# Kernel optimization log

Measured on AMD Instinct MI355X. Metric: run time of the kernel, lower is better.

The kernel has to match this reference:

```python
import jax, jax.numpy as jnp
import numpy as np
from math import sqrt

N_HEADS = 4
IN_FEATURES = 64
KQ = 64
HEAD_V = IN_FEATURES // N_HEADS  # 16


def setup_inputs() -> dict:
    key = jax.random.key(0)
    ks = jax.random.split(key, 7)
    s = 0.05
    x = jax.random.normal(ks[0], (8192, IN_FEATURES), dtype=jnp.float32)
    # Per-head Linear weights stacked on a leading head axis.
    # torch Linear: y = x @ W.T + b; we store W already transposed: [H, F, E]
    Wq = jax.random.normal(ks[1], (N_HEADS, IN_FEATURES, KQ), dtype=jnp.float32) * s
    bq = jax.random.normal(ks[2], (N_HEADS, KQ), dtype=jnp.float32) * s
    Wk = jax.random.normal(ks[3], (N_HEADS, IN_FEATURES, KQ), dtype=jnp.float32) * s
    bk = jax.random.normal(ks[4], (N_HEADS, KQ), dtype=jnp.float32) * s
    Wv = jax.random.normal(ks[5], (N_HEADS, IN_FEATURES, HEAD_V), dtype=jnp.float32) * s
    bv = jax.random.normal(ks[6], (N_HEADS, HEAD_V), dtype=jnp.float32) * s
    return {"x": x, "Wq": Wq, "bq": bq, "Wk": Wk, "bk": bk, "Wv": Wv, "bv": bv}


def reference(x, Wq, bq, Wk, bk, Wv, bv):
    N, F = x.shape
    scale = 1.0 / sqrt(F)  # original divides by sqrt(in_features), NOT sqrt(kq)
    # Batched-head projections: [H, N, E]
    Q = jnp.einsum('nf,hfe->hne', x, Wq) + bq[:, None, :]
    K = jnp.einsum('nf,hfe->hne', x, Wk) + bk[:, None, :]
    V = jnp.einsum('nf,hfd->hnd', x, Wv) + bv[:, None, :]
    logits = jnp.einsum('hne,hme->hnm', Q, K) * scale  # [H, N, N]
    attn = jax.nn.softmax(logits, axis=-1)
    out_heads = jnp.einsum('hnm,hmd->hnd', attn, V)    # [H, N, HEAD_V]
    # Head i writes columns [i*HEAD_V:(i+1)*HEAD_V] of the output.
    out = jnp.transpose(out_heads, (1, 0, 2)).reshape(N, F)
    return out
```

## Files before the change

kernel.cpp:

```cpp
#include <hip/hip_runtime.h>

typedef __attribute__((ext_vector_type(4))) float f32x4;
typedef __attribute__((ext_vector_type(8))) short bf16x8;
typedef __attribute__((ext_vector_type(4))) short bf16x4;
typedef long fp8x8;

#define NH 4

static __device__ __forceinline__ unsigned short f2bf(float f){
  unsigned u = __float_as_uint(f);
  u += 0x7FFFu + ((u >> 16) & 1u);
  return (unsigned short)(u >> 16);
}

static __device__ __forceinline__ unsigned pack2bf(float a, float b){
  return __builtin_amdgcn_perm(__float_as_uint(b) + 0x8000u,
                               __float_as_uint(a) + 0x8000u, 0x07060302u);
}

static __device__ __forceinline__ unsigned pack2bf_t(float a, float b){
  return __builtin_amdgcn_perm(__float_as_uint(b), __float_as_uint(a), 0x07060302u);
}

static __device__ __forceinline__ int pack_fp8x4(float a, float b, float c, float d){
  int w = __builtin_amdgcn_cvt_pk_fp8_f32(a, b, 0, false);
  w     = __builtin_amdgcn_cvt_pk_fp8_f32(c, d, w, true);
  return w;
}

__global__ __launch_bounds__(256) void wprep_kernel(
    const float* __restrict__ Wq, const float* __restrict__ bq,
    const float* __restrict__ Wk, const float* __restrict__ bk,
    const float* __restrict__ Wv,
    unsigned short* __restrict__ WF, float* __restrict__ bias_s, int n)
{
  __shared__ unsigned short wqT[64*72];
  __shared__ unsigned short wkT[64*72];
  __shared__ unsigned short wvT[16*72];

  const int t = threadIdx.x;
  const int h = blockIdx.x;
  const float S1 = 0.4246609001f;
  const int f = t >> 2, eg = t & 3;

  {
    const float4* g = (const float4*)(Wq + h*4096 + f*64 + eg*16);
    #pragma unroll
    for (int p = 0; p < 4; ++p){
      float4 d = g[p];
      int e0 = eg*16 + p*4;
      wqT[(e0+0)*72 + f] = f2bf(d.x * S1);
      wqT[(e0+1)*72 + f] = f2bf(d.y * S1);
      wqT[(e0+2)*72 + f] = f2bf(d.z * S1);
      wqT[(e0+3)*72 + f] = f2bf(d.w * S1);
    }
  }
  {
    const float4* g = (const float4*)(Wk + h*4096 + f*64 + eg*16);
    #pragma unroll
    for (int p = 0; p < 4; ++p){
      float4 d = g[p];
      int e0 = eg*16 + p*4;
      wkT[(e0+0)*72 + f] = f2bf(d.x * S1);
      wkT[(e0+1)*72 + f] = f2bf(d.y * S1);
      wkT[(e0+2)*72 + f] = f2bf(d.z * S1);
      wkT[(e0+3)*72 + f] = f2bf(d.w * S1);
    }
  }
  {
    float4 d = *(const float4*)(Wv + h*1024 + f*16 + eg*4);
    int d0 = eg*4;
    wvT[(d0+0)*72 + f] = f2bf(d.x);
    wvT[(d0+1)*72 + f] = f2bf(d.y);
    wvT[(d0+2)*72 + f] = f2bf(d.z);
    wvT[(d0+3)*72 + f] = f2bf(d.w);
  }
  if (t < 64)       bias_s[h*128 + t] = bq[h*64 + t] * S1;
  else if (t < 128) bias_s[h*128 + t] = bk[h*64 + (t-64)] * S1;
  __syncthreads();

  const int lane = t & 63, w = t >> 6;
  const int quad = lane >> 4, l16 = lane & 15;
  for (int s = w; s < 18; s += 4){
    const unsigned short* src;
    if (s < 8){      int et = s>>1,     ks = s&1;     src = wqT + (et*16+l16)*72 + ks*32 + quad*8; }
    else if (s < 16){int ft = (s-8)>>1, ks = (s-8)&1; src = wkT + (ft*16+l16)*72 + ks*32 + quad*8; }
    else {           int ks = s-16;                   src = wvT + l16*72 + ks*32 + quad*8; }
    uint4 v = *(const uint4*)src;
    *(uint4*)(WF + ((size_t)(h*18 + s)*64 + lane)*8) = v;
  }
}

__global__ __launch_bounds__(256) void proj_kernel(
    const float* __restrict__ x, const float* __restrict__ bv,
    const unsigned short* __restrict__ WF, const float* __restrict__ bias_s,
    unsigned char* __restrict__ Qfr, unsigned char* __restrict__ Kt,
    unsigned short* __restrict__ Vt, int n)
{
  __shared__ unsigned short xf[8*64*8];
  __shared__ float bql[64], bkl[64], bvl[16];

  const int t  = threadIdx.x;
  const int h  = blockIdx.y;
  const int r0 = blockIdx.x * 64;

  {
    const int r = t >> 2, cg4 = t & 3;
    const float4* g = (const float4*)(x + (size_t)(r0 + r)*64 + cg4*16);
    float4 a = g[0], b = g[1], c = g[2], d = g[3];
    unsigned u0 = pack2bf(a.x,a.y), u1 = pack2bf(a.z,a.w);
    unsigned u2 = pack2bf(b.x,b.y), u3 = pack2bf(b.z,b.w);
    unsigned u4 = pack2bf(c.x,c.y), u5 = pack2bf(c.z,c.w);
    unsigned u6 = pack2bf(d.x,d.y), u7 = pack2bf(d.z,d.w);
    const int it = r >> 4, l16r = r & 15, ks = cg4 >> 1, q0 = (cg4 & 1)*2;
    uint4* dst0 = (uint4*)(xf + ((it*2+ks)*64 + q0*16     + l16r)*8);
    uint4* dst1 = (uint4*)(xf + ((it*2+ks)*64 + (q0+1)*16 + l16r)*8);
    *dst0 = make_uint4(u0,u1,u2,u3);
    *dst1 = make_uint4(u4,u5,u6,u7);
  }
  if (t < 64)        bql[t]     = bias_s[h*128 + t];
  else if (t < 128)  bkl[t-64]  = bias_s[h*128 + t];
  else if (t < 144)  bvl[t-128] = bv[h*16 + (t-128)];
  __syncthreads();

  const int lane = t & 63, w = t >> 6;
  const int quad = lane >> 4, l16 = lane & 15;

  bf16x8 xa[8];
  #pragma unroll
  for (int i = 0; i < 8; ++i)
    xa[i] = *(const bf16x8*)(xf + (i*64 + lane)*8);

  const unsigned short* WFh = WF + (size_t)h*18*64*8;
  bf16x8 wq0 = *(const bf16x8*)(WFh + ((size_t)(     w*2 + 0)*64 + lane)*8);
  bf16x8 wq1 = *(const bf16x8*)(WFh + ((size_t)(     w*2 + 1)*64 + lane)*8);
  bf16x8 wk0 = *(const bf16x8*)(WFh + ((size_t)(8  + w*2 + 0)*64 + lane)*8);
  bf16x8 wk1 = *(const bf16x8*)(WFh + ((size_t)(8  + w*2 + 1)*64 + lane)*8);
  bf16x8 wv0 = *(const bf16x8*)(WFh + ((size_t)16*64 + lane)*8);
  bf16x8 wv1 = *(const bf16x8*)(WFh + ((size_t)17*64 + lane)*8);

  const f32x4 z = {0.f,0.f,0.f,0.f};
  f32x4 accQ[4] = {z,z,z,z};
  f32x4 accK[4] = {z,z,z,z};
  f32x4 accV = z;

  #pragma unroll
  for (int it = 0; it < 4; ++it){
    accQ[it] = __builtin_amdgcn_mfma_f32_16x16x32_bf16(wq0, xa[it*2+0], accQ[it], 0,0,0);
    accQ[it] = __builtin_amdgcn_mfma_f32_16x16x32_bf16(wq1, xa[it*2+1], accQ[it], 0,0,0);
  }
  #pragma unroll
  for (int tt = 0; tt < 4; ++tt){
    accK[tt] = __builtin_amdgcn_mfma_f32_16x16x32_bf16(wk0, xa[tt*2+0], accK[tt], 0,0,0);
    accK[tt] = __builtin_amdgcn_mfma_f32_16x16x32_bf16(wk1, xa[tt*2+1], accK[tt], 0,0,0);
  }
  accV = __builtin_amdgcn_mfma_f32_16x16x32_bf16(xa[w*2+0], wv0, accV, 0,0,0);
  accV = __builtin_amdgcn_mfma_f32_16x16x32_bf16(xa[w*2+1], wv1, accV, 0,0,0);

  {
    const int e0 = w*16 + quad*4;
    const float b0 = bql[e0], b1 = bql[e0+1], b2 = bql[e0+2], b3 = bql[e0+3];
    const int qk = (e0 & 31) >> 3, hf = e0 >> 5, boff = (quad & 1) * 4;
    #pragma unroll
    for (int it = 0; it < 4; ++it){
      unsigned o = pack_fp8x4(accQ[it][0]+b0, accQ[it][1]+b1,
                              accQ[it][2]+b2, accQ[it][3]+b3);
      const int T = (r0 >> 4) + it;
      *(unsigned*)(Qfr + (size_t)h*((size_t)n<<6) + (size_t)T*1024
                       + (qk*16 + l16)*16 + hf*8 + boff) = o;
    }
  }
  {
    const int f0 = w*16 + quad*4;
    const float bk0 = bkl[f0], bk1 = bkl[f0+1], bk2 = bkl[f0+2], bk3 = bkl[f0+3];
    const int qk = (f0 & 31) >> 3, hf = f0 >> 5, boff = (quad & 1) * 4;
    #pragma unroll
    for (int tt = 0; tt < 4; ++tt){
      unsigned o = pack_fp8x4(accK[tt][0]+bk0, accK[tt][1]+bk1,
                              accK[tt][2]+bk2, accK[tt][3]+bk3);
      const int T = (r0 >> 4) + tt;
      *(unsigned*)(Kt + (size_t)h*((size_t)n<<6) + (size_t)T*1024
                      + (qk*16 + l16)*16 + hf*8 + boff) = o;
    }
  }
  {
    float bvv = bvl[l16];
    unsigned v01 = pack2bf(accV[0]+bvv, accV[1]+bvv);
    unsigned v23 = pack2bf(accV[2]+bvv, accV[3]+bvv);
    const int T = (r0 >> 4) + w;
    *(uint2*)(Vt + (size_t)h*((size_t)n<<4) + ((size_t)T*64 + lane)*4) = make_uint2(v01, v23);
  }
}

__global__ __launch_bounds__(512, 8) void attn_kernel(
    const unsigned char* __restrict__ Qfr, const unsigned char* __restrict__ Kt,
    const unsigned short* __restrict__ Vt, float* __restrict__ out, int n)
{
  __shared__ float part[7][64][17];

  const int tid  = threadIdx.x;
  const int lane = tid & 63;
  const int jq   = tid >> 6;
  const int bid  = blockIdx.x;
  const int h    = bid & 3;
  const int iblk = bid >> 2;
  const int l16  = lane & 15, quad = lane >> 4;
  const int i0   = iblk*32;
  const int ntq  = (n >> 3) >> 4;
  const int tile0 = jq * ntq;

  const unsigned char* qfh = Qfr + (size_t)h*((size_t)n<<6);
  longlong2 q0 = *(const longlong2*)(qfh + (size_t)((i0>>4)    )*1024 + lane*16);
  longlong2 q1 = *(const longlong2*)(qfh + (size_t)((i0>>4) + 1)*1024 + lane*16);
  const fp8x8 qf00 = (fp8x8)q0.x;
  const fp8x8 qf01 = (fp8x8)q0.y;
  const fp8x8 qf10 = (fp8x8)q1.x;
  const fp8x8 qf11 = (fp8x8)q1.y;

  const longlong2* ktl = (const longlong2*)(Kt + (size_t)h*((size_t)n<<6)) + (size_t)tile0*64 + lane;
  const uint2*     vtu = (const uint2*)(Vt + (size_t)h*((size_t)n<<4)) + (size_t)tile0*64 + lane;

  f32x4 o0  = {0.f,0.f,0.f,0.f};
  f32x4 o1  = {0.f,0.f,0.f,0.f};
  f32x4 la0 = {0.f,0.f,0.f,0.f};
  f32x4 la1 = {0.f,0.f,0.f,0.f};
  const f32x4 z = {0.f,0.f,0.f,0.f};
  const bf16x4 vones = {(short)0x3F80, (short)0x3F80, (short)0x3F80, (short)0x3F80};

  longlong2 ka = ktl[0];
  uint2     va = vtu[0];
  longlong2 kb = ktl[64];
  uint2     vb = vtu[64];

#define ATTN_TILE(KK, VV)                                                     \
  {                                                                           \
    fp8x8 k0 = (fp8x8)KK.x;                                                   \
    fp8x8 k1 = (fp8x8)KK.y;                                                   \
    bf16x4 vf; { union { uint2 u; bf16x4 v; } c; c.u = VV; vf = c.v; }        \
    f32x4 s0 = __builtin_amdgcn_mfma_f32_16x16x32_fp8_fp8(k0, qf00, z, 0,0,0);\
    s0 = __builtin_amdgcn_mfma_f32_16x16x32_fp8_fp8(k1, qf01, s0, 0,0,0);     \
    f32x4 s1 = __builtin_amdgcn_mfma_f32_16x16x32_fp8_fp8(k0, qf10, z, 0,0,0);\
    s1 = __builtin_amdgcn_mfma_f32_16x16x32_fp8_fp8(k1, qf11, s1, 0,0,0);     \
    float p00 = __builtin_amdgcn_exp2f(s0[0]);                                \
    float p01 = __builtin_amdgcn_exp2f(s0[1]);                                \
    float p02 = __builtin_amdgcn_exp2f(s0[2]);                                \
    float p03 = __builtin_amdgcn_exp2f(s0[3]);                                \
    float p10 = __builtin_amdgcn_exp2f(s1[0]);                                \
    float p11 = __builtin_amdgcn_exp2f(s1[1]);                                \
    float p12 = __builtin_amdgcn_exp2f(s1[2]);                                \
    float p13 = __builtin_amdgcn_exp2f(s1[3]);                                \
    union { uint2 u; bf16x4 v; } pc0, pc1;                                    \
    pc0.u = make_uint2(pack2bf_t(p00,p01), pack2bf_t(p02,p03));               \
    pc1.u = make_uint2(pack2bf_t(p10,p11), pack2bf_t(p12,p13));               \
    o0  = __builtin_amdgcn_mfma_f32_16x16x16bf16_1k(pc0.v, vf,    o0,  0,0,0);\
    o1  = __builtin_amdgcn_mfma_f32_16x16x16bf16_1k(pc1.v, vf,    o1,  0,0,0);\
    la0 = __builtin_amdgcn_mfma_f32_16x16x16bf16_1k(pc0.v, vones, la0, 0,0,0);\
    la1 = __builtin_amdgcn_mfma_f32_16x16x16bf16_1k(pc1.v, vones, la1, 0,0,0);\
  }

  for (int tt = 0; tt < ntq - 2; tt += 2){
    longlong2 kc = ktl[128];
    uint2     vc = vtu[128];
    longlong2 kd = ktl[192];
    uint2     vd = vtu[192];
    ATTN_TILE(ka, va)
    ATTN_TILE(kb, vb)
    ka = kc; va = vc;
    kb = kd; vb = vd;
    ktl += 128; vtu += 128;
  }
  ATTN_TILE(ka, va)
  ATTN_TILE(kb, vb)
#undef ATTN_TILE

  if (jq > 0){
    float* p = &part[jq-1][lane][0];
    p[ 0]=o0[0];  p[ 1]=o0[1];  p[ 2]=o0[2];  p[ 3]=o0[3];
    p[ 4]=o1[0];  p[ 5]=o1[1];  p[ 6]=o1[2];  p[ 7]=o1[3];
    p[ 8]=la0[0]; p[ 9]=la0[1]; p[10]=la0[2]; p[11]=la0[3];
    p[12]=la1[0]; p[13]=la1[1]; p[14]=la1[2]; p[15]=la1[3];
  }
  __syncthreads();

  if (jq == 0){
    #pragma unroll
    for (int q = 0; q < 7; ++q){
      const float* r = &part[q][lane][0];
      o0[0] +=r[0];  o0[1] +=r[1];  o0[2] +=r[2];  o0[3] +=r[3];
      o1[0] +=r[4];  o1[1] +=r[5];  o1[2] +=r[6];  o1[3] +=r[7];
      la0[0]+=r[8];  la0[1]+=r[9];  la0[2]+=r[10]; la0[3]+=r[11];
      la1[0]+=r[12]; la1[1]+=r[13]; la1[2]+=r[14]; la1[3]+=r[15];
    }
    #pragma unroll
    for (int reg = 0; reg < 4; ++reg){
      int i = quad*4 + reg;
      out[(size_t)(i0 + i)*64      + h*16 + l16] = o0[reg] / la0[reg];
      out[(size_t)(i0 + 16 + i)*64 + h*16 + l16] = o1[reg] / la1[reg];
    }
  }
}

extern "C" void kernel_launch(void* const* d_in, const int* in_sizes, int n_in,
                              void* d_out, int out_size, void* d_ws, size_t ws_size,
                              hipStream_t stream) {
  const float* x  = (const float*)d_in[0];
  const float* Wq = (const float*)d_in[1];
  const float* bq = (const float*)d_in[2];
  const float* Wk = (const float*)d_in[3];
  const float* bk = (const float*)d_in[4];
  const float* Wv = (const float*)d_in[5];
  const float* bv = (const float*)d_in[6];
  float* out = (float*)d_out;

  const int n = in_sizes[0] / 64;

  unsigned char* Qfr  = (unsigned char*)d_ws;
  unsigned char* Kt   = Qfr + (size_t)NH*n*64;
  unsigned short* Vt  = (unsigned short*)(Kt + (size_t)NH*n*64);
  unsigned short* WF  = Vt + (size_t)NH*n*16;
  float* bias_s       = (float*)(WF + (size_t)NH*18*64*8);

  wprep_kernel<<<NH, 256, 0, stream>>>(Wq, bq, Wk, bk, Wv, WF, bias_s, n);
  proj_kernel<<<dim3(n/64, NH), 256, 0, stream>>>(x, bv, WF, bias_s, Qfr, Kt, Vt, n);
  attn_kernel<<<dim3((n/32)*NH), 512, 0, stream>>>(Qfr, Kt, Vt, out, n);
}
```

Measured before the change: 122.4 us.

## Use 16x16x32 bf16 MFMA for PV by pairing key tiles with interleaved V layout

Stores V so that two consecutive 16-key tiles sit interleaved in one 16-byte per-lane chunk. The attention loop now handles two key tiles per step and issues the PV and row-sum products with the K=32 bf16 MFMA instead of two K=16 MFMAs. This halves the PV/rowsum MFMA instruction count and widens the V loads. It also relaxes launch bounds from 8 to 4 waves-per-EU minimum, which allows more registers per thread but may reduce occupancy. Prefetch depth in the loop changes to match the chunked schedule.

```diff
diff --git a/kernel.cpp b/kernel.cpp
--- a/kernel.cpp
+++ b/kernel.cpp
@@ -188,11 +188,12 @@
     unsigned v01 = pack2bf(accV[0]+bvv, accV[1]+bvv);
     unsigned v23 = pack2bf(accV[2]+bvv, accV[3]+bvv);
     const int T = (r0 >> 4) + w;
-    *(uint2*)(Vt + (size_t)h*((size_t)n<<4) + ((size_t)T*64 + lane)*4) = make_uint2(v01, v23);
-  }
-}
-
-__global__ __launch_bounds__(512, 8) void attn_kernel(
+    *(uint2*)(Vt + (size_t)h*((size_t)n<<4)
+                 + ((size_t)(T>>1)*64 + lane)*8 + (T&1)*4) = make_uint2(v01, v23);
+  }
+}
+
+__global__ __launch_bounds__(512, 4) void attn_kernel(
     const unsigned char* __restrict__ Qfr, const unsigned char* __restrict__ Kt,
     const unsigned short* __restrict__ Vt, float* __restrict__ out, int n)
 {
@@ -207,6 +208,7 @@
   const int l16  = lane & 15, quad = lane >> 4;
   const int i0   = iblk*32;
   const int ntq  = (n >> 3) >> 4;
+  const int nch  = ntq >> 1;
   const int tile0 = jq * ntq;
 
   const unsigned char* qfh = Qfr + (size_t)h*((size_t)n<<6);
@@ -218,60 +220,74 @@
   const fp8x8 qf11 = (fp8x8)q1.y;
 
   const longlong2* ktl = (const longlong2*)(Kt + (size_t)h*((size_t)n<<6)) + (size_t)tile0*64 + lane;
-  const uint2*     vtu = (const uint2*)(Vt + (size_t)h*((size_t)n<<4)) + (size_t)tile0*64 + lane;
+  const uint4*     vtu = (const uint4*)(Vt + (size_t)h*((size_t)n<<4)) + (size_t)(tile0>>1)*64 + lane;
 
   f32x4 o0  = {0.f,0.f,0.f,0.f};
   f32x4 o1  = {0.f,0.f,0.f,0.f};
   f32x4 la0 = {0.f,0.f,0.f,0.f};
   f32x4 la1 = {0.f,0.f,0.f,0.f};
   const f32x4 z = {0.f,0.f,0.f,0.f};
-  const bf16x4 vones = {(short)0x3F80, (short)0x3F80, (short)0x3F80, (short)0x3F80};
-
-  longlong2 ka = ktl[0];
-  uint2     va = vtu[0];
-  longlong2 kb = ktl[64];
-  uint2     vb = vtu[64];
-
-#define ATTN_TILE(KK, VV)                                                     \
+  const bf16x8 vones = {(short)0x3F80, (short)0x3F80, (short)0x3F80, (short)0x3F80,
+                        (short)0x3F80, (short)0x3F80, (short)0x3F80, (short)0x3F80};
+
+  longlong2 ka0 = ktl[0],   ka1 = ktl[64];
+  uint4     va  = vtu[0];
+  longlong2 kb0 = ktl[128], kb1 = ktl[192];
+  uint4     vb  = vtu[64];
+
+#define ATTN_CHUNK(KA, KB, VV)                                                \
   {                                                                           \
-    fp8x8 k0 = (fp8x8)KK.x;                                                   \
-    fp8x8 k1 = (fp8x8)KK.y;                                                   \
-    bf16x4 vf; { union { uint2 u; bf16x4 v; } c; c.u = VV; vf = c.v; }        \
-    f32x4 s0 = __builtin_amdgcn_mfma_f32_16x16x32_fp8_fp8(k0, qf00, z, 0,0,0);\
-    s0 = __builtin_amdgcn_mfma_f32_16x16x32_fp8_fp8(k1, qf01, s0, 0,0,0);     \
-    f32x4 s1 = __builtin_amdgcn_mfma_f32_16x16x32_fp8_fp8(k0, qf10, z, 0,0,0);\
-    s1 = __builtin_amdgcn_mfma_f32_16x16x32_fp8_fp8(k1, qf11, s1, 0,0,0);     \
-    float p00 = __builtin_amdgcn_exp2f(s0[0]);                                \
-    float p01 = __builtin_amdgcn_exp2f(s0[1]);                                \
-    float p02 = __builtin_amdgcn_exp2f(s0[2]);                                \
-    float p03 = __builtin_amdgcn_exp2f(s0[3]);                                \
-    float p10 = __builtin_amdgcn_exp2f(s1[0]);                                \
-    float p11 = __builtin_amdgcn_exp2f(s1[1]);                                \
-    float p12 = __builtin_amdgcn_exp2f(s1[2]);                                \
-    float p13 = __builtin_amdgcn_exp2f(s1[3]);                                \
-    union { uint2 u; bf16x4 v; } pc0, pc1;                                    \
-    pc0.u = make_uint2(pack2bf_t(p00,p01), pack2bf_t(p02,p03));               \
-    pc1.u = make_uint2(pack2bf_t(p10,p11), pack2bf_t(p12,p13));               \
-    o0  = __builtin_amdgcn_mfma_f32_16x16x16bf16_1k(pc0.v, vf,    o0,  0,0,0);\
-    o1  = __builtin_amdgcn_mfma_f32_16x16x16bf16_1k(pc1.v, vf,    o1,  0,0,0);\
-    la0 = __builtin_amdgcn_mfma_f32_16x16x16bf16_1k(pc0.v, vones, la0, 0,0,0);\
-    la1 = __builtin_amdgcn_mfma_f32_16x16x16bf16_1k(pc1.v, vones, la1, 0,0,0);\
-  }
-
-  for (int tt = 0; tt < ntq - 2; tt += 2){
-    longlong2 kc = ktl[128];
-    uint2     vc = vtu[128];
-    longlong2 kd = ktl[192];
-    uint2     vd = vtu[192];
-    ATTN_TILE(ka, va)
-    ATTN_TILE(kb, vb)
-    ka = kc; va = vc;
-    kb = kd; vb = vd;
-    ktl += 128; vtu += 128;
-  }
-  ATTN_TILE(ka, va)
-  ATTN_TILE(kb, vb)
-#undef ATTN_TILE
+    fp8x8 a0 = (fp8x8)KA.x;                                                   \
+    fp8x8 a1 = (fp8x8)KA.y;                                                   \
+    fp8x8 b0 = (fp8x8)KB.x;                                                   \
+    fp8x8 b1 = (fp8x8)KB.y;                                                   \
+    f32x4 s0 = __builtin_amdgcn_mfma_f32_16x16x32_fp8_fp8(a0, qf00, z, 0,0,0);\
+    s0 = __builtin_amdgcn_mfma_f32_16x16x32_fp8_fp8(a1, qf01, s0, 0,0,0);     \
+    f32x4 s1 = __builtin_amdgcn_mfma_f32_16x16x32_fp8_fp8(a0, qf10, z, 0,0,0);\
+    s1 = __builtin_amdgcn_mfma_f32_16x16x32_fp8_fp8(a1, qf11, s1, 0,0,0);     \
+    f32x4 t0 = __builtin_amdgcn_mfma_f32_16x16x32_fp8_fp8(b0, qf00, z, 0,0,0);\
+    t0 = __builtin_amdgcn_mfma_f32_16x16x32_fp8_fp8(b1, qf01, t0, 0,0,0);     \
+    f32x4 t1 = __builtin_amdgcn_mfma_f32_16x16x32_fp8_fp8(b0, qf10, z, 0,0,0);\
+    t1 = __builtin_amdgcn_mfma_f32_16x16x32_fp8_fp8(b1, qf11, t1, 0,0,0);     \
+    float pa00 = __builtin_amdgcn_exp2f(s0[0]);                               \
+    float pa01 = __builtin_amdgcn_exp2f(s0[1]);                               \
+    float pa02 = __builtin_amdgcn_exp2f(s0[2]);                               \
+    float pa03 = __builtin_amdgcn_exp2f(s0[3]);                               \
+    float pa10 = __builtin_amdgcn_exp2f(s1[0]);                               \
+    float pa11 = __builtin_amdgcn_exp2f(s1[1]);                               \
+    float pa12 = __builtin_amdgcn_exp2f(s1[2]);                               \
+    float pa13 = __builtin_amdgcn_exp2f(s1[3]);                               \
+    float pb00 = __builtin_amdgcn_exp2f(t0[0]);                               \
+    float pb01 = __builtin_amdgcn_exp2f(t0[1]);                               \
+    float pb02 = __builtin_amdgcn_exp2f(t0[2]);                               \
+    float pb03 = __builtin_amdgcn_exp2f(t0[3]);                               \
+    float pb10 = __builtin_amdgcn_exp2f(t1[0]);                               \
+    float pb11 = __builtin_amdgcn_exp2f(t1[1]);                               \
+    float pb12 = __builtin_amdgcn_exp2f(t1[2]);                               \
+    float pb13 = __builtin_amdgcn_exp2f(t1[3]);                               \
+    union { uint4 u; bf16x8 v; } pq0, pq1, vfu;                               \
+    pq0.u = make_uint4(pack2bf_t(pa00,pa01), pack2bf_t(pa02,pa03),            \
+                       pack2bf_t(pb00,pb01), pack2bf_t(pb02,pb03));           \
+    pq1.u = make_uint4(pack2bf_t(pa10,pa11), pack2bf_t(pa12,pa13),            \
+                       pack2bf_t(pb10,pb11), pack2bf_t(pb12,pb13));           \
+    vfu.u = VV;                                                               \
+    o0  = __builtin_amdgcn_mfma_f32_16x16x32_bf16(pq0.v, vfu.v, o0,  0,0,0);  \
+    o1  = __builtin_amdgcn_mfma_f32_16x16x32_bf16(pq1.v, vfu.v, o1,  0,0,0);  \
+    la0 = __builtin_amdgcn_mfma_f32_16x16x32_bf16(pq0.v, vones, la0, 0,0,0);  \
+    la1 = __builtin_amdgcn_mfma_f32_16x16x32_bf16(pq1.v, vones, la1, 0,0,0);  \
+  }
+
+  for (int c = 0; c < nch - 2; ++c){
+    longlong2 kc0 = ktl[256], kc1 = ktl[320];
+    uint4     vc  = vtu[128];
+    ATTN_CHUNK(ka0, ka1, va)
+    ka0 = kb0; ka1 = kb1; va = vb;
+    kb0 = kc0; kb1 = kc1; vb = vc;
+    ktl += 128; vtu += 64;
+  }
+  ATTN_CHUNK(ka0, ka1, va)
+  ATTN_CHUNK(kb0, kb1, vb)
+#undef ATTN_CHUNK
 
   if (jq > 0){
     float* p = &part[jq-1][lane][0];
```

New measurement: 120.8 us. No clear change (-1.3%).

## Split attention into MFMA and exp2 warp roles with LDS ping-pong pipeline

Applied to the files above, without the earlier changes.

Attention is restructured into warp specialization. Four waves run the QK fp8 MFMAs and the PV bf16 MFMAs, and four other waves run exp2 and bf16 packing. Scores and probabilities pass between them through double-buffered, swizzled LDS with a block barrier each chunk. V is stored interleaved so PV can use the 16x16x32 bf16 MFMA. Occupancy hint drops from 8 to 4 and the cross-wave reduction shrinks to 2 partials. The goal is to overlap transcendental work with matrix work, at the cost of per-chunk __syncthreads and LDS traffic.

```diff
diff --git a/kernel.cpp b/kernel.cpp
--- a/kernel.cpp
+++ b/kernel.cpp
@@ -2,7 +2,6 @@
 
 typedef __attribute__((ext_vector_type(4))) float f32x4;
 typedef __attribute__((ext_vector_type(8))) short bf16x8;
-typedef __attribute__((ext_vector_type(4))) short bf16x4;
 typedef long fp8x8;
 
 #define NH 4
@@ -188,114 +187,139 @@
     unsigned v01 = pack2bf(accV[0]+bvv, accV[1]+bvv);
     unsigned v23 = pack2bf(accV[2]+bvv, accV[3]+bvv);
     const int T = (r0 >> 4) + w;
-    *(uint2*)(Vt + (size_t)h*((size_t)n<<4) + ((size_t)T*64 + lane)*4) = make_uint2(v01, v23);
-  }
-}
-
-__global__ __launch_bounds__(512, 8) void attn_kernel(
+    *(uint2*)(Vt + (size_t)h*((size_t)n<<4)
+                 + ((size_t)(T>>1)*64 + lane)*8 + (T&1)*4) = make_uint2(v01, v23);
+  }
+}
+
+__global__ __launch_bounds__(512, 4) void attn_kernel(
     const unsigned char* __restrict__ Qfr, const unsigned char* __restrict__ Kt,
     const unsigned short* __restrict__ Vt, float* __restrict__ out, int n)
 {
-  __shared__ float part[7][64][17];
+  __shared__ char xbuf[16384 + 8192];
+  __shared__ float part[2][64][9];
+
+  char* sbv = xbuf;
+  char* pbv = xbuf + 16384;
 
   const int tid  = threadIdx.x;
   const int lane = tid & 63;
-  const int jq   = tid >> 6;
+  const int w    = tid >> 6;
+  const bool mw  = (w < 4);
+  const int p    = w & 3;
+  const int rh   = p & 1;
+  const int kh   = p >> 1;
+
   const int bid  = blockIdx.x;
   const int h    = bid & 3;
   const int iblk = bid >> 2;
   const int l16  = lane & 15, quad = lane >> 4;
   const int i0   = iblk*32;
-  const int ntq  = (n >> 3) >> 4;
-  const int tile0 = jq * ntq;
-
-  const unsigned char* qfh = Qfr + (size_t)h*((size_t)n<<6);
-  longlong2 q0 = *(const longlong2*)(qfh + (size_t)((i0>>4)    )*1024 + lane*16);
-  longlong2 q1 = *(const longlong2*)(qfh + (size_t)((i0>>4) + 1)*1024 + lane*16);
-  const fp8x8 qf00 = (fp8x8)q0.x;
-  const fp8x8 qf01 = (fp8x8)q0.y;
-  const fp8x8 qf10 = (fp8x8)q1.x;
-  const fp8x8 qf11 = (fp8x8)q1.y;
-
-  const longlong2* ktl = (const longlong2*)(Kt + (size_t)h*((size_t)n<<6)) + (size_t)tile0*64 + lane;
-  const uint2*     vtu = (const uint2*)(Vt + (size_t)h*((size_t)n<<4)) + (size_t)tile0*64 + lane;
-
-  f32x4 o0  = {0.f,0.f,0.f,0.f};
-  f32x4 o1  = {0.f,0.f,0.f,0.f};
-  f32x4 la0 = {0.f,0.f,0.f,0.f};
-  f32x4 la1 = {0.f,0.f,0.f,0.f};
+  const int nch  = n >> 6;
+  const int tile0 = kh * (n >> 5);
+
+  const int swz = (lane*16) ^ (((lane>>3)&3) << 4);
+  char* sbp = sbv + p*2048 + swz;
+  char* pbp = pbv + p*1024 + swz;
+
   const f32x4 z = {0.f,0.f,0.f,0.f};
-  const bf16x4 vones = {(short)0x3F80, (short)0x3F80, (short)0x3F80, (short)0x3F80};
-
-  longlong2 ka = ktl[0];
-  uint2     va = vtu[0];
-  longlong2 kb = ktl[64];
-  uint2     vb = vtu[64];
-
-#define ATTN_TILE(KK, VV)                                                     \
-  {                                                                           \
-    fp8x8 k0 = (fp8x8)KK.x;                                                   \
-    fp8x8 k1 = (fp8x8)KK.y;                                                   \
-    bf16x4 vf; { union { uint2 u; bf16x4 v; } c; c.u = VV; vf = c.v; }        \
-    f32x4 s0 = __builtin_amdgcn_mfma_f32_16x16x32_fp8_fp8(k0, qf00, z, 0,0,0);\
-    s0 = __builtin_amdgcn_mfma_f32_16x16x32_fp8_fp8(k1, qf01, s0, 0,0,0);     \
-    f32x4 s1 = __builtin_amdgcn_mfma_f32_16x16x32_fp8_fp8(k0, qf10, z, 0,0,0);\
-    s1 = __builtin_amdgcn_mfma_f32_16x16x32_fp8_fp8(k1, qf11, s1, 0,0,0);     \
-    float p00 = __builtin_amdgcn_exp2f(s0[0]);                                \
-    float p01 = __builtin_amdgcn_exp2f(s0[1]);                                \
-    float p02 = __builtin_amdgcn_exp2f(s0[2]);                                \
-    float p03 = __builtin_amdgcn_exp2f(s0[3]);                                \
-    float p10 = __builtin_amdgcn_exp2f(s1[0]);                                \
-    float p11 = __builtin_amdgcn_exp2f(s1[1]);                                \
-    float p12 = __builtin_amdgcn_exp2f(s1[2]);                                \
-    float p13 = __builtin_amdgcn_exp2f(s1[3]);                                \
-    union { uint2 u; bf16x4 v; } pc0, pc1;                                    \
-    pc0.u = make_uint2(pack2bf_t(p00,p01), pack2bf_t(p02,p03));               \
-    pc1.u = make_uint2(pack2bf_t(p10,p11), pack2bf_t(p12,p13));               \
-    o0  = __builtin_amdgcn_mfma_f32_16x16x16bf16_1k(pc0.v, vf,    o0,  0,0,0);\
-    o1  = __builtin_amdgcn_mfma_f32_16x16x16bf16_1k(pc1.v, vf,    o1,  0,0,0);\
-    la0 = __builtin_amdgcn_mfma_f32_16x16x16bf16_1k(pc0.v, vones, la0, 0,0,0);\
-    la1 = __builtin_amdgcn_mfma_f32_16x16x16bf16_1k(pc1.v, vones, la1, 0,0,0);\
-  }
-
-  for (int tt = 0; tt < ntq - 2; tt += 2){
-    longlong2 kc = ktl[128];
-    uint2     vc = vtu[128];
-    longlong2 kd = ktl[192];
-    uint2     vd = vtu[192];
-    ATTN_TILE(ka, va)
-    ATTN_TILE(kb, vb)
-    ka = kc; va = vc;
-    kb = kd; vb = vd;
-    ktl += 128; vtu += 128;
-  }
-  ATTN_TILE(ka, va)
-  ATTN_TILE(kb, vb)
-#undef ATTN_TILE
-
-  if (jq > 0){
-    float* p = &part[jq-1][lane][0];
-    p[ 0]=o0[0];  p[ 1]=o0[1];  p[ 2]=o0[2];  p[ 3]=o0[3];
-    p[ 4]=o1[0];  p[ 5]=o1[1];  p[ 6]=o1[2];  p[ 7]=o1[3];
-    p[ 8]=la0[0]; p[ 9]=la0[1]; p[10]=la0[2]; p[11]=la0[3];
-    p[12]=la1[0]; p[13]=la1[1]; p[14]=la1[2]; p[15]=la1[3];
+  const bf16x8 vones = {(short)0x3F80, (short)0x3F80, (short)0x3F80, (short)0x3F80,
+                        (short)0x3F80, (short)0x3F80, (short)0x3F80, (short)0x3F80};
+
+  fp8x8 qf0 = 0, qf1 = 0;
+  longlong2 kcA, kcB;
+  uint4 vPrev, vCur;
+  const longlong2* ktl = nullptr;
+  const uint4*     vtu = nullptr;
+  f32x4 o = z, la = z;
+
+  if (mw){
+    const unsigned char* qfh = Qfr + (size_t)h*((size_t)n<<6);
+    longlong2 q = *(const longlong2*)(qfh + (size_t)((i0>>4)+rh)*1024 + lane*16);
+    qf0 = (fp8x8)q.x; qf1 = (fp8x8)q.y;
+    ktl = (const longlong2*)(Kt + (size_t)h*((size_t)n<<6)) + (size_t)tile0*64 + lane;
+    vtu = (const uint4*)(Vt + (size_t)h*((size_t)n<<4)) + (size_t)(tile0>>1)*64 + lane;
+    kcA = ktl[0]; kcB = ktl[64];
+    vCur = vtu[0];
+    vPrev = vCur;
+  }
+
+  for (int c = 0; c < nch; ++c){
+    if (mw){
+      const fp8x8 a0 = (fp8x8)kcA.x, a1 = (fp8x8)kcA.y;
+      const fp8x8 b0 = (fp8x8)kcB.x, b1 = (fp8x8)kcB.y;
+      f32x4 s = __builtin_amdgcn_mfma_f32_16x16x32_fp8_fp8(a0, qf0, z, 0,0,0);
+      s = __builtin_amdgcn_mfma_f32_16x16x32_fp8_fp8(a1, qf1, s, 0,0,0);
+      f32x4 u = __builtin_amdgcn_mfma_f32_16x16x32_fp8_fp8(b0, qf0, z, 0,0,0);
+      u = __builtin_amdgcn_mfma_f32_16x16x32_fp8_fp8(b1, qf1, u, 0,0,0);
+      *(f32x4*)(sbp + (c&1)*8192       ) = s;
+      *(f32x4*)(sbp + (c&1)*8192 + 1024) = u;
+      kcA = ktl[128]; kcB = ktl[192]; ktl += 128;
+    } else if (c > 0){
+      f32x4 s = *(const f32x4*)(sbp + ((c-1)&1)*8192       );
+      f32x4 u = *(const f32x4*)(sbp + ((c-1)&1)*8192 + 1024);
+      float e0 = __builtin_amdgcn_exp2f(s[0]);
+      float e1 = __builtin_amdgcn_exp2f(s[1]);
+      float e2 = __builtin_amdgcn_exp2f(s[2]);
+      float e3 = __builtin_amdgcn_exp2f(s[3]);
+      float f0 = __builtin_amdgcn_exp2f(u[0]);
+      float f1 = __builtin_amdgcn_exp2f(u[1]);
+      float f2 = __builtin_amdgcn_exp2f(u[2]);
+      float f3 = __builtin_amdgcn_exp2f(u[3]);
+      uint4 pq = make_uint4(pack2bf_t(e0,e1), pack2bf_t(e2,e3),
+                            pack2bf_t(f0,f1), pack2bf_t(f2,f3));
+      *(uint4*)(pbp + ((c-1)&1)*4096) = pq;
+    }
+    __syncthreads();
+    if (mw){
+      if (c > 0){
+        union { uint4 uu; bf16x8 v; } pq; pq.uu = *(const uint4*)(pbp + ((c-1)&1)*4096);
+        union { uint4 uu; bf16x8 v; } vf; vf.uu = vPrev;
+        o  = __builtin_amdgcn_mfma_f32_16x16x32_bf16(pq.v, vf.v,  o,  0,0,0);
+        la = __builtin_amdgcn_mfma_f32_16x16x32_bf16(pq.v, vones, la, 0,0,0);
+      }
+      vPrev = vCur; vCur = vtu[64]; vtu += 64;
+    }
+  }
+  if (!mw){
+    const int b = (nch-1)&1;
+    f32x4 s = *(const f32x4*)(sbp + b*8192       );
+    f32x4 u = *(const f32x4*)(sbp + b*8192 + 1024);
+    float e0 = __builtin_amdgcn_exp2f(s[0]);
+    float e1 = __builtin_amdgcn_exp2f(s[1]);
+    float e2 = __builtin_amdgcn_exp2f(s[2]);
+    float e3 = __builtin_amdgcn_exp2f(s[3]);
+    float f0 = __builtin_amdgcn_exp2f(u[0]);
+    float f1 = __builtin_amdgcn_exp2f(u[1]);
+    float f2 = __builtin_amdgcn_exp2f(u[2]);
+    float f3 = __builtin_amdgcn_exp2f(u[3]);
+    uint4 pq = make_uint4(pack2bf_t(e0,e1), pack2bf_t(e2,e3),
+                          pack2bf_t(f0,f1), pack2bf_t(f2,f3));
+    *(uint4*)(pbp + b*4096) = pq;
   }
   __syncthreads();
-
-  if (jq == 0){
-    #pragma unroll
-    for (int q = 0; q < 7; ++q){
-      const float* r = &part[q][lane][0];
-      o0[0] +=r[0];  o0[1] +=r[1];  o0[2] +=r[2];  o0[3] +=r[3];
-      o1[0] +=r[4];  o1[1] +=r[5];  o1[2] +=r[6];  o1[3] +=r[7];
-      la0[0]+=r[8];  la0[1]+=r[9];  la0[2]+=r[10]; la0[3]+=r[11];
-      la1[0]+=r[12]; la1[1]+=r[13]; la1[2]+=r[14]; la1[3]+=r[15];
-    }
+  if (mw){
+    const int b = (nch-1)&1;
+    union { uint4 uu; bf16x8 v; } pq; pq.uu = *(const uint4*)(pbp + b*4096);
+    union { uint4 uu; bf16x8 v; } vf; vf.uu = vPrev;
+    o  = __builtin_amdgcn_mfma_f32_16x16x32_bf16(pq.v, vf.v,  o,  0,0,0);
+    la = __builtin_amdgcn_mfma_f32_16x16x32_bf16(pq.v, vones, la, 0,0,0);
+  }
+
+  if (mw && kh == 1){
+    float* q = &part[rh][lane][0];
+    q[0]=o[0];  q[1]=o[1];  q[2]=o[2];  q[3]=o[3];
+    q[4]=la[0]; q[5]=la[1]; q[6]=la[2]; q[7]=la[3];
+  }
+  __syncthreads();
+  if (mw && kh == 0){
+    const float* q = &part[rh][lane][0];
+    o[0] +=q[0]; o[1] +=q[1]; o[2] +=q[2]; o[3] +=q[3];
+    la[0]+=q[4]; la[1]+=q[5]; la[2]+=q[6]; la[3]+=q[7];
     #pragma unroll
     for (int reg = 0; reg < 4; ++reg){
-      int i = quad*4 + reg;
-      out[(size_t)(i0 + i)*64      + h*16 + l16] = o0[reg] / la0[reg];
-      out[(size_t)(i0 + 16 + i)*64 + h*16 + l16] = o1[reg] / la1[reg];
+      int i = rh*16 + quad*4 + reg;
+      out[(size_t)(i0 + i)*64 + h*16 + l16] = o[reg] / la[reg];
     }
   }
 }
```

After: 161.6 us. 1.32x slower.
